# Performance work log

Measured on AMD Instinct MI355X. Metric: run time of the kernel, lower is better.

The kernel has to match this reference:

```python
import jax, jax.numpy as jnp
import numpy as np

# dims: batch B, seq S, model D, query heads H, kv heads KV, head_dim HD, group G
B, S, D = 2, 2048, 2048
H, KV, HD = 16, 4, 128
G = H // KV
THETA = 10000.0


def setup_inputs() -> dict:
    key = jax.random.key(0)
    ks = jax.random.split(key, 5)
    x = jax.random.normal(ks[0], (B, S, D), dtype=jnp.float32)
    # RoPE frequencies (real/imag parts of complex freqs_cis)
    inv_freq = 1.0 / (THETA ** (jnp.arange(0, HD, 2, dtype=jnp.float32) / HD))  # (HD/2,)
    t = jnp.arange(S, dtype=jnp.float32)
    freqs = jnp.outer(t, inv_freq)                      # (S, HD/2)
    freqs_cos = jnp.cos(freqs)
    freqs_sin = jnp.sin(freqs)
    # causal additive mask
    mask = jnp.where(jnp.tril(jnp.ones((S, S), dtype=bool)), 0.0, -1e9).astype(jnp.float32)
    sc = 0.02
    wq = jax.random.normal(ks[1], (D, H * HD), dtype=jnp.float32) * sc
    wk = jax.random.normal(ks[2], (D, KV * HD), dtype=jnp.float32) * sc
    wv = jax.random.normal(ks[3], (D, KV * HD), dtype=jnp.float32) * sc
    wo = jax.random.normal(ks[4], (H * HD, D), dtype=jnp.float32) * sc
    return {"x": x, "freqs_cos": freqs_cos, "freqs_sin": freqs_sin, "mask": mask,
            "wq": wq, "wk": wk, "wv": wv, "wo": wo}


def _apply_rope(x, cos, sin):
    # x: (B, S, nh, HD); cos/sin: (S, HD/2). Interleaved complex rotation.
    xr = x.reshape(*x.shape[:-1], HD // 2, 2)
    xe, xo = xr[..., 0], xr[..., 1]
    c = cos[None, :, None, :]
    s = sin[None, :, None, :]
    out_e = xe * c - xo * s
    out_o = xe * s + xo * c
    return jnp.stack([out_e, out_o], axis=-1).reshape(x.shape)


def reference(x, freqs_cos, freqs_sin, mask, wq, wk, wv, wo):
    q = (x @ wq).reshape(B, S, H, HD)
    k = (x @ wk).reshape(B, S, KV, HD)
    v = (x @ wv).reshape(B, S, KV, HD)
    q = _apply_rope(q, freqs_cos, freqs_sin)
    k = _apply_rope(k, freqs_cos, freqs_sin)
    # GQA: group query heads instead of expanding KV (same math as expand)
    qg = q.reshape(B, S, KV, G, HD)
    scale = jnp.sqrt(jnp.float32(HD))
    scores = jnp.einsum('bqkgd,bskd->bkgqs', qg, k) / scale   # (B,KV,G,S,S)
    scores = scores + mask                                     # broadcast (S,S)
    attn = jax.nn.softmax(scores, axis=-1)
    out = jnp.einsum('bkgqs,bskd->bqkgd', attn, v)             # (B,S,KV,G,HD)
    out = out.reshape(B, S, H * HD)
    return out @ wo
```

## Files before the change

### kernel.cpp

```cpp
#include <hip/hip_runtime.h>
#include <type_traits>

typedef short s8v   __attribute__((ext_vector_type(8)));
typedef float f32x4 __attribute__((ext_vector_type(4)));
typedef float f32x16 __attribute__((ext_vector_type(16)));
typedef unsigned int u32x2 __attribute__((ext_vector_type(2)));
typedef unsigned int u32x4 __attribute__((ext_vector_type(4)));

__device__ __forceinline__ unsigned short f2bf(float f) {
    unsigned int u = __builtin_bit_cast(unsigned int, f);
    u += 0x7FFF + ((u >> 16) & 1);
    return (unsigned short)(u >> 16);
}
__device__ __forceinline__ float bf2f(unsigned short b) {
    unsigned int u = ((unsigned int)b) << 16;
    return __builtin_bit_cast(float, u);
}
__device__ __forceinline__ unsigned int cvtpk(float lo, float hi) {
    unsigned int w;
    asm("v_cvt_pk_bf16_f32 %0, %1, %2" : "=v"(w) : "v"(lo), "v"(hi));
    return w;
}

__device__ __forceinline__ void gload16(const void* g, void* l) {
    __builtin_amdgcn_global_load_lds(
        (const __attribute__((address_space(1))) void*)g,
        (__attribute__((address_space(3))) void*)l, 16, 0, 0);
}

__global__ __launch_bounds__(256)
void prep_kernel(const float* __restrict__ x, const float* __restrict__ wq,
                 const float* __restrict__ wk, const float* __restrict__ wv,
                 const float* __restrict__ wo,
                 unsigned short* __restrict__ xb, unsigned short* __restrict__ wqkvT,
                 unsigned short* __restrict__ woT) {
    __shared__ float tile[32][33];
    const int bid = blockIdx.x;
    if (bid < 4096) {
        int i = bid * 256 + threadIdx.x;
        const f32x4* s4 = (const f32x4*)x;
        f32x4 a = s4[2 * i], b = s4[2 * i + 1];
        s8v o;
        o[0] = (short)f2bf(a[0]); o[1] = (short)f2bf(a[1]);
        o[2] = (short)f2bf(a[2]); o[3] = (short)f2bf(a[3]);
        o[4] = (short)f2bf(b[0]); o[5] = (short)f2bf(b[1]);
        o[6] = (short)f2bf(b[2]); o[7] = (short)f2bf(b[3]);
        *(s8v*)(xb + (size_t)i * 8) = o;
        return;
    }
    const int tx = threadIdx.x & 31, ty = threadIdx.x >> 5;
    const float* src; unsigned short* dst; int sc, N, n0, k0;
    if (bid < 10240) {
        int lb = bid - 4096;
        n0 = (lb % 96) * 32; k0 = (lb / 96) * 32;
        if (n0 < 2048)      { src = wq; sc = n0;        N = 2048; }
        else if (n0 < 2560) { src = wk; sc = n0 - 2048; N = 512;  }
        else                { src = wv; sc = n0 - 2560; N = 512;  }
        dst = wqkvT;
    } else {
        int lb = bid - 10240;
        n0 = (lb % 64) * 32; k0 = (lb / 64) * 32;
        src = wo; sc = n0; N = 2048; dst = woT;
    }
#pragma unroll
    for (int r = 0; r < 4; ++r)
        tile[ty + r * 8][tx] = src[(size_t)(k0 + ty + r * 8) * N + sc + tx];
    __syncthreads();
#pragma unroll
    for (int r = 0; r < 4; ++r)
        dst[(size_t)(n0 + ty + r * 8) * 2048 + k0 + tx] = f2bf(tile[tx][ty + r * 8]);
}

__global__ void rope_kernel(unsigned short* __restrict__ qkv,
                            const float* __restrict__ fc, const float* __restrict__ fs) {
    int idx = blockIdx.x * blockDim.x + threadIdx.x;
    if (idx >= 4096 * 20 * 16) return;
    int grp = idx & 15;
    int hh = (idx >> 4) % 20;
    int row = idx / (16 * 20);
    int s = row & 2047;
    int col0 = (hh < 16 ? hh * 128 : 2048 + (hh - 16) * 128) + grp * 8;
    unsigned short* p = qkv + (size_t)row * 3072 + col0;
    s8v v = *(const s8v*)p;
    const float* cc = fc + (size_t)s * 64 + grp * 4;
    const float* ss = fs + (size_t)s * 64 + grp * 4;
    const float sc = (hh < 16) ? 0.08838834764831845f : 1.0f;
#pragma unroll
    for (int j = 0; j < 4; ++j) {
        float xe = bf2f((unsigned short)v[2 * j]);
        float xo = bf2f((unsigned short)v[2 * j + 1]);
        float c = cc[j], sn = ss[j];
        v[2 * j]     = (short)f2bf((xe * c - xo * sn) * sc);
        v[2 * j + 1] = (short)f2bf((xe * sn + xo * c) * sc);
    }
    *(s8v*)p = v;
}

__global__ void vtrans(const unsigned short* __restrict__ qkv, unsigned short* __restrict__ vt) {
    __shared__ unsigned short t[32][33];
    int s0 = blockIdx.x * 32;
    int c0 = blockIdx.y * 32;
    int tx = threadIdx.x, ty = threadIdx.y;
#pragma unroll
    for (int r = 0; r < 4; ++r)
        t[ty + r * 8][tx] = qkv[(size_t)(s0 + ty + r * 8) * 3072 + 2560 + c0 + tx];
    __syncthreads();
    int b = s0 >> 11, s = s0 & 2047;
    size_t dbase = (size_t)(b * 4 + (c0 >> 7)) * 128 + (c0 & 127);
#pragma unroll
    for (int r = 0; r < 4; ++r)
        vt[(dbase + ty + r * 8) * 2048 + s + tx] = t[tx][ty + r * 8];
}

template <typename CT>
__global__ __launch_bounds__(256)
void gemm_bt(const unsigned short* __restrict__ A, const unsigned short* __restrict__ BT,
             CT* __restrict__ C, int M, int N, int K, int ldc) {
    __shared__ unsigned short As[128 * 64];
    __shared__ unsigned short Bs[128 * 64];
    const int tid = threadIdx.x;
    const int wid = tid >> 6, lane = tid & 63;
    const int l31 = lane & 31, h2 = lane >> 5;
    const int nbx = N >> 7;
    const int per = nbx >> 3;
    const int xcd = blockIdx.x & 7;
    const int li  = blockIdx.x >> 3;
    const int bx  = xcd * per + (li % per);
    const int by  = li / per;
    const int brow = by * 128, bcol = bx * 128;
    const int wr = wid >> 1, wc = wid & 1;
    f32x16 acc[2][2] = {};

    for (int kt = 0; kt < K; kt += 64) {
#pragma unroll
        for (int i = 0; i < 4; ++i) {
            int c = i * 256 + tid;
            int row = c >> 3, u = c & 7;
            gload16(A + (size_t)(brow + row) * K + kt + ((u ^ (row & 7)) << 3),
                    As + (size_t)c * 8);
            gload16(BT + (size_t)(bcol + row) * K + kt + ((u ^ (row & 7)) << 3),
                    Bs + (size_t)c * 8);
        }
        __syncthreads();
        s8v a[2][4], b[2][4];
#pragma unroll
        for (int mm = 0; mm < 2; ++mm) {
            int row = wr * 64 + mm * 32 + l31;
#pragma unroll
            for (int ks = 0; ks < 4; ++ks)
                a[mm][ks] = *(const s8v*)(As + (size_t)row * 64 +
                                          (((2 * ks + h2) ^ (row & 7)) << 3));
        }
#pragma unroll
        for (int nn = 0; nn < 2; ++nn) {
            int row = wc * 64 + nn * 32 + l31;
#pragma unroll
            for (int ks = 0; ks < 4; ++ks)
                b[nn][ks] = *(const s8v*)(Bs + (size_t)row * 64 +
                                          (((2 * ks + h2) ^ (row & 7)) << 3));
        }
#pragma unroll
        for (int ks = 0; ks < 4; ++ks)
#pragma unroll
            for (int mm = 0; mm < 2; ++mm)
#pragma unroll
                for (int nn = 0; nn < 2; ++nn)
                    acc[mm][nn] = __builtin_amdgcn_mfma_f32_32x32x16_bf16(
                        a[mm][ks], b[nn][ks], acc[mm][nn], 0, 0, 0);
        __syncthreads();
    }
#pragma unroll
    for (int mm = 0; mm < 2; ++mm)
#pragma unroll
        for (int nn = 0; nn < 2; ++nn)
#pragma unroll
            for (int reg = 0; reg < 16; ++reg) {
                int r = brow + wr * 64 + mm * 32 + (reg & 3) + 8 * (reg >> 2) + 4 * h2;
                int c = bcol + wc * 64 + nn * 32 + l31;
                float v = acc[mm][nn][reg];
                if constexpr (std::is_same<CT, float>::value)
                    C[(size_t)r * ldc + c] = v;
                else
                    C[(size_t)r * ldc + c] = f2bf(v);
            }
}

__global__ __launch_bounds__(256)
void attn_kernel(const unsigned short* __restrict__ qkv,
                 const unsigned short* __restrict__ vtg,
                 unsigned short* __restrict__ out) {
    constexpr int S = 2048;
    __shared__ unsigned short Ks[2][64 * 128];
    __shared__ unsigned short Vs[2][128 * 64];
    const int tid = threadIdx.x, lane = tid & 63, wid = tid >> 6;
    const int l31 = lane & 31, h2 = lane >> 5;
    const int lsw = l31 & 7;
    const int g8 = blockIdx.x & 7;
    const int b = g8 >> 2, kvh = g8 & 3;
    const int qi = 63 - (blockIdx.x >> 3);
    const int h = kvh * 4 + wid;
    const int qw = qi * 32;
    const int qq = qw + l31;
    const size_t rs = 3072;

    const unsigned short* Qp = qkv + (size_t)(b * S + qw) * rs + h * 128 + h2 * 8;
    const unsigned short* Kbase = qkv + (size_t)(b * S) * rs + 2048 + kvh * 128;
    const unsigned short* Vtg = vtg + (size_t)((b * 4 + kvh) * 128) * S;

    s8v qf[8];
#pragma unroll
    for (int kk = 0; kk < 8; ++kk)
        qf[kk] = *(const s8v*)(Qp + (size_t)l31 * rs + kk * 16);

    f32x16 acc[4] = {};
    float m_run = -1e30f, l_run = 0.f;
    const int nt = (qi >> 1) + 1;

    auto stage = [&](int t, int bufi) {
        const int kb64 = t * 64;
#pragma unroll
        for (int i = 0; i < 4; ++i) {
            int c = i * 256 + tid;
            int key = c >> 4, d8 = c & 15;
            gload16(Kbase + (size_t)(kb64 + key) * rs + ((d8 ^ (key & 7)) << 3),
                    &Ks[bufi][(size_t)c * 8]);
        }
#pragma unroll
        for (int i = 0; i < 4; ++i) {
            int c = i * 256 + tid;
            int d = c >> 3, k8 = c & 7;
            gload16(Vtg + (size_t)d * S + kb64 + ((k8 ^ (d & 7)) << 3),
                    &Vs[bufi][(size_t)c * 8]);
        }
    };

    int cur = 0;
    stage(0, 0);
    __syncthreads();

    for (int t = 0; t < nt; ++t) {
        if (t + 1 < nt) stage(t + 1, cur ^ 1);
        const int kb64 = t * 64;
        const char* Kb = (const char*)&Ks[cur][0];
        const char* Vb = (const char*)&Vs[cur][0];

        s8v kf0[8], kf1[8];
#pragma unroll
        for (int kk = 0; kk < 8; ++kk)
            kf0[kk] = *(const s8v*)(Kb + l31 * 256 + (((2 * kk + h2) ^ lsw) << 4));
#pragma unroll
        for (int kk = 0; kk < 8; ++kk)
            kf1[kk] = *(const s8v*)(Kb + (32 + l31) * 256 + (((2 * kk + h2) ^ lsw) << 4));
        s8v vf[4][4];
#pragma unroll
        for (int kb = 0; kb < 4; ++kb)
#pragma unroll
            for (int dblk = 0; dblk < 4; ++dblk)
                vf[kb][dblk] = *(const s8v*)(Vb + (32 * dblk + l31) * 128 +
                                             (((2 * kb + h2) ^ lsw) << 4));

        f32x16 sacc0 = {}, sacc1 = {};
        __builtin_amdgcn_s_setprio(1);
#pragma unroll
        for (int kk = 0; kk < 8; ++kk)
            sacc0 = __builtin_amdgcn_mfma_f32_32x32x16_bf16(kf0[kk], qf[kk], sacc0, 0, 0, 0);
#pragma unroll
        for (int kk = 0; kk < 8; ++kk)
            sacc1 = __builtin_amdgcn_mfma_f32_32x32x16_bf16(kf1[kk], qf[kk], sacc1, 0, 0, 0);
        __builtin_amdgcn_s_setprio(0);

        float sv[32];
        if (t == nt - 1) {
#pragma unroll
            for (int g = 0; g < 2; ++g)
#pragma unroll
                for (int r = 0; r < 16; ++r) {
                    int key = kb64 + 32 * g + (r & 3) + 8 * (r >> 2) + 4 * h2;
                    float s = (g ? sacc1[r] : sacc0[r]);
                    sv[g * 16 + r] = (key <= qq) ? s : -1e30f;
                }
        } else {
#pragma unroll
            for (int r = 0; r < 16; ++r) sv[r] = sacc0[r];
#pragma unroll
            for (int r = 0; r < 16; ++r) sv[16 + r] = sacc1[r];
        }

        float mx = sv[0];
#pragma unroll
        for (int i = 1; i < 32; ++i) mx = fmaxf(mx, sv[i]);
        mx = fmaxf(mx, __shfl_xor(mx, 32));
        if (!__all(mx - m_run <= 8.f)) {
            float mn = fmaxf(m_run, mx);
            float alpha = __expf(m_run - mn);
            m_run = mn;
            l_run *= alpha;
#pragma unroll
            for (int dblk = 0; dblk < 4; ++dblk)
#pragma unroll
                for (int r = 0; r < 16; ++r) acc[dblk][r] *= alpha;
        }
        float ps = 0.f;
#pragma unroll
        for (int i = 0; i < 32; ++i) {
            float e = __expf(sv[i] - m_run);
            sv[i] = e;
            ps += e;
        }
        ps += __shfl_xor(ps, 32);
        l_run += ps;

        unsigned int pw[4][4];
#pragma unroll
        for (int g = 0; g < 2; ++g) {
            unsigned int w[8];
#pragma unroll
            for (int j = 0; j < 8; ++j)
                w[j] = cvtpk(sv[g * 16 + 2 * j], sv[g * 16 + 2 * j + 1]);
#pragma unroll
            for (int u = 0; u < 2; ++u) {
                unsigned int t0 = (unsigned)__shfl_xor((int)w[4 * u + 0], 32);
                unsigned int t1 = (unsigned)__shfl_xor((int)w[4 * u + 1], 32);
                unsigned int t2 = (unsigned)__shfl_xor((int)w[4 * u + 2], 32);
                unsigned int t3 = (unsigned)__shfl_xor((int)w[4 * u + 3], 32);
                pw[2 * g + u][0] = h2 ? t2 : w[4 * u + 0];
                pw[2 * g + u][1] = h2 ? t3 : w[4 * u + 1];
                pw[2 * g + u][2] = h2 ? w[4 * u + 2] : t0;
                pw[2 * g + u][3] = h2 ? w[4 * u + 3] : t1;
            }
        }

        __builtin_amdgcn_s_setprio(1);
#pragma unroll
        for (int kb = 0; kb < 4; ++kb) {
            u32x4 wv;
            wv[0] = pw[kb][0]; wv[1] = pw[kb][1]; wv[2] = pw[kb][2]; wv[3] = pw[kb][3];
            s8v pf = __builtin_bit_cast(s8v, wv);
#pragma unroll
            for (int dblk = 0; dblk < 4; ++dblk)
                acc[dblk] = __builtin_amdgcn_mfma_f32_32x32x16_bf16(vf[kb][dblk], pf, acc[dblk], 0, 0, 0);
        }
        __builtin_amdgcn_s_setprio(0);

        __syncthreads();
        cur ^= 1;
    }

    float inv = 1.f / l_run;
    unsigned short* Op = out + (size_t)(b * S + qq) * 2048 + h * 128 + 4 * h2;
#pragma unroll
    for (int dblk = 0; dblk < 4; ++dblk)
#pragma unroll
        for (int s = 0; s < 4; ++s) {
            u32x2 wv;
            wv[0] = cvtpk(acc[dblk][4 * s + 0] * inv, acc[dblk][4 * s + 1] * inv);
            wv[1] = cvtpk(acc[dblk][4 * s + 2] * inv, acc[dblk][4 * s + 3] * inv);
            *(u32x2*)(Op + 32 * dblk + 8 * s) = wv;
        }
}

extern "C" void kernel_launch(void* const* d_in, const int* in_sizes, int n_in,
                              void* d_out, int out_size, void* d_ws, size_t ws_size,
                              hipStream_t stream) {
    const float* x  = (const float*)d_in[0];
    const float* fc = (const float*)d_in[1];
    const float* fs = (const float*)d_in[2];
    const float* wq = (const float*)d_in[4];
    const float* wk = (const float*)d_in[5];
    const float* wv = (const float*)d_in[6];
    const float* wo = (const float*)d_in[7];
    float* out = (float*)d_out;

    char* ws = (char*)d_ws;
    unsigned short* xb    = (unsigned short*)ws;
    unsigned short* wqkvT = (unsigned short*)(ws + 16777216);
    unsigned short* woT   = (unsigned short*)(ws + 16777216 + 12582912);
    unsigned short* qkvb  = (unsigned short*)(ws + 16777216 + 12582912 + 8388608);
    unsigned short* attnb = xb;
    unsigned short* vtb   = wqkvT;

    prep_kernel<<<14336, 256, 0, stream>>>(x, wq, wk, wv, wo, xb, wqkvT, woT);
    gemm_bt<unsigned short><<<768, 256, 0, stream>>>(
        xb, wqkvT, qkvb, 4096, 3072, 2048, 3072);
    rope_kernel<<<5120, 256, 0, stream>>>(qkvb, fc, fs);
    dim3 tb(32, 8);
    vtrans<<<dim3(128, 16), tb, 0, stream>>>(qkvb, vtb);
    attn_kernel<<<512, 256, 0, stream>>>(qkvb, vtb, attnb);
    gemm_bt<float><<<512, 256, 0, stream>>>(
        attnb, woT, out, 4096, 2048, 2048, 2048);
}
```

Measured before the change: 220.8 us.

## Split long causal attention blocks across KV, merge partials, fuse RoPE with V transpose

Query blocks in the upper half of the causal range have their KV loop split into two halves, each run by a separate block. Those blocks write unnormalized fp32 partial outputs plus (max, sum) pairs into scratch, and a new merge kernel combines the two halves. The aim is to fix load imbalance, since the longest query blocks otherwise dominate the attention tail. RoPE and the V transpose now run in one launch to save a kernel launch. Softmax switches to exp2 with log2(e) folded into the Q scale, and the rescale threshold is widened. This costs an extra kernel and extra fp32 scratch traffic, reusing the output buffer as scratch.

After: 256.0 us. 15.9% more time.

```diff
diff --git a/kernel.cpp b/kernel.cpp
--- a/kernel.cpp
+++ b/kernel.cpp
@@ -71,36 +71,37 @@
         dst[(size_t)(n0 + ty + r * 8) * 2048 + k0 + tx] = f2bf(tile[tx][ty + r * 8]);
 }
 
-__global__ void rope_kernel(unsigned short* __restrict__ qkv,
-                            const float* __restrict__ fc, const float* __restrict__ fs) {
-    int idx = blockIdx.x * blockDim.x + threadIdx.x;
-    if (idx >= 4096 * 20 * 16) return;
-    int grp = idx & 15;
-    int hh = (idx >> 4) % 20;
-    int row = idx / (16 * 20);
-    int s = row & 2047;
-    int col0 = (hh < 16 ? hh * 128 : 2048 + (hh - 16) * 128) + grp * 8;
-    unsigned short* p = qkv + (size_t)row * 3072 + col0;
-    s8v v = *(const s8v*)p;
-    const float* cc = fc + (size_t)s * 64 + grp * 4;
-    const float* ss = fs + (size_t)s * 64 + grp * 4;
-    const float sc = (hh < 16) ? 0.08838834764831845f : 1.0f;
-#pragma unroll
-    for (int j = 0; j < 4; ++j) {
-        float xe = bf2f((unsigned short)v[2 * j]);
-        float xo = bf2f((unsigned short)v[2 * j + 1]);
-        float c = cc[j], sn = ss[j];
-        v[2 * j]     = (short)f2bf((xe * c - xo * sn) * sc);
-        v[2 * j + 1] = (short)f2bf((xe * sn + xo * c) * sc);
-    }
-    *(s8v*)p = v;
-}
-
-__global__ void vtrans(const unsigned short* __restrict__ qkv, unsigned short* __restrict__ vt) {
+__global__ __launch_bounds__(256)
+void ropevt_kernel(unsigned short* __restrict__ qkv, const float* __restrict__ fc,
+                   const float* __restrict__ fs, unsigned short* __restrict__ vt) {
     __shared__ unsigned short t[32][33];
-    int s0 = blockIdx.x * 32;
-    int c0 = blockIdx.y * 32;
-    int tx = threadIdx.x, ty = threadIdx.y;
+    const int bid = blockIdx.x;
+    if (bid < 5120) {
+        int idx = bid * 256 + threadIdx.x;
+        int grp = idx & 15;
+        int hh = (idx >> 4) % 20;
+        int row = idx / (16 * 20);
+        int s = row & 2047;
+        int col0 = (hh < 16 ? hh * 128 : 2048 + (hh - 16) * 128) + grp * 8;
+        unsigned short* p = qkv + (size_t)row * 3072 + col0;
+        s8v v = *(const s8v*)p;
+        const float* cc = fc + (size_t)s * 64 + grp * 4;
+        const float* ss = fs + (size_t)s * 64 + grp * 4;
+        const float sc = (hh < 16) ? (0.08838834764831845f * 1.4426950408889634f) : 1.0f;
+#pragma unroll
+        for (int j = 0; j < 4; ++j) {
+            float xe = bf2f((unsigned short)v[2 * j]);
+            float xo = bf2f((unsigned short)v[2 * j + 1]);
+            float c = cc[j], sn = ss[j];
+            v[2 * j]     = (short)f2bf((xe * c - xo * sn) * sc);
+            v[2 * j + 1] = (short)f2bf((xe * sn + xo * c) * sc);
+        }
+        *(s8v*)p = v;
+        return;
+    }
+    int vb = bid - 5120;
+    int s0 = (vb & 127) * 32, c0 = (vb >> 7) * 32;
+    int tx = threadIdx.x & 31, ty = threadIdx.x >> 5;
 #pragma unroll
     for (int r = 0; r < 4; ++r)
         t[ty + r * 8][tx] = qkv[(size_t)(s0 + ty + r * 8) * 3072 + 2560 + c0 + tx];
@@ -188,16 +189,29 @@
 __global__ __launch_bounds__(256)
 void attn_kernel(const unsigned short* __restrict__ qkv,
                  const unsigned short* __restrict__ vtg,
-                 unsigned short* __restrict__ out) {
+                 unsigned short* __restrict__ out,
+                 float* __restrict__ opart, float* __restrict__ ml) {
     constexpr int S = 2048;
     __shared__ unsigned short Ks[2][64 * 128];
     __shared__ unsigned short Vs[2][128 * 64];
     const int tid = threadIdx.x, lane = tid & 63, wid = tid >> 6;
     const int l31 = lane & 31, h2 = lane >> 5;
     const int lsw = l31 & 7;
-    const int g8 = blockIdx.x & 7;
+
+    const int u = blockIdx.x;
+    int qi, g8, t0, t1, half = 0, split = 0;
+    if (u < 512) {
+        int pair = u >> 1; half = u & 1; split = 1;
+        qi = 63 - (pair >> 3); g8 = pair & 7;
+        int ntf0 = (qi >> 1) + 1, nth = ntf0 >> 1;
+        t0 = half ? nth : 0; t1 = half ? ntf0 : nth;
+    } else {
+        int v2 = u - 512;
+        qi = 31 - (v2 >> 3); g8 = v2 & 7;
+        t0 = 0; t1 = (qi >> 1) + 1;
+    }
+    const int ntf = (qi >> 1) + 1;
     const int b = g8 >> 2, kvh = g8 & 3;
-    const int qi = 63 - (blockIdx.x >> 3);
     const int h = kvh * 4 + wid;
     const int qw = qi * 32;
     const int qq = qw + l31;
@@ -214,7 +228,6 @@
 
     f32x16 acc[4] = {};
     float m_run = -1e30f, l_run = 0.f;
-    const int nt = (qi >> 1) + 1;
 
     auto stage = [&](int t, int bufi) {
         const int kb64 = t * 64;
@@ -235,11 +248,11 @@
     };
 
     int cur = 0;
-    stage(0, 0);
+    stage(t0, 0);
     __syncthreads();
 
-    for (int t = 0; t < nt; ++t) {
-        if (t + 1 < nt) stage(t + 1, cur ^ 1);
+    for (int t = t0; t < t1; ++t) {
+        if (t + 1 < t1) stage(t + 1, cur ^ 1);
         const int kb64 = t * 64;
         const char* Kb = (const char*)&Ks[cur][0];
         const char* Vb = (const char*)&Vs[cur][0];
@@ -270,7 +283,7 @@
         __builtin_amdgcn_s_setprio(0);
 
         float sv[32];
-        if (t == nt - 1) {
+        if (t == ntf - 1) {
 #pragma unroll
             for (int g = 0; g < 2; ++g)
 #pragma unroll
@@ -290,9 +303,9 @@
 #pragma unroll
         for (int i = 1; i < 32; ++i) mx = fmaxf(mx, sv[i]);
         mx = fmaxf(mx, __shfl_xor(mx, 32));
-        if (!__all(mx - m_run <= 8.f)) {
+        if (!__all(mx - m_run <= 11.5f)) {
             float mn = fmaxf(m_run, mx);
-            float alpha = __expf(m_run - mn);
+            float alpha = exp2f(m_run - mn);
             m_run = mn;
             l_run *= alpha;
 #pragma unroll
@@ -303,7 +316,7 @@
         float ps = 0.f;
 #pragma unroll
         for (int i = 0; i < 32; ++i) {
-            float e = __expf(sv[i] - m_run);
+            float e = exp2f(sv[i] - m_run);
             sv[i] = e;
             ps += e;
         }
@@ -318,15 +331,15 @@
             for (int j = 0; j < 8; ++j)
                 w[j] = cvtpk(sv[g * 16 + 2 * j], sv[g * 16 + 2 * j + 1]);
 #pragma unroll
-            for (int u = 0; u < 2; ++u) {
-                unsigned int t0 = (unsigned)__shfl_xor((int)w[4 * u + 0], 32);
-                unsigned int t1 = (unsigned)__shfl_xor((int)w[4 * u + 1], 32);
-                unsigned int t2 = (unsigned)__shfl_xor((int)w[4 * u + 2], 32);
-                unsigned int t3 = (unsigned)__shfl_xor((int)w[4 * u + 3], 32);
-                pw[2 * g + u][0] = h2 ? t2 : w[4 * u + 0];
-                pw[2 * g + u][1] = h2 ? t3 : w[4 * u + 1];
-                pw[2 * g + u][2] = h2 ? w[4 * u + 2] : t0;
-                pw[2 * g + u][3] = h2 ? w[4 * u + 3] : t1;
+            for (int uu = 0; uu < 2; ++uu) {
+                unsigned int t0w = (unsigned)__shfl_xor((int)w[4 * uu + 0], 32);
+                unsigned int t1w = (unsigned)__shfl_xor((int)w[4 * uu + 1], 32);
+                unsigned int t2w = (unsigned)__shfl_xor((int)w[4 * uu + 2], 32);
+                unsigned int t3w = (unsigned)__shfl_xor((int)w[4 * uu + 3], 32);
+                pw[2 * g + uu][0] = h2 ? t2w : w[4 * uu + 0];
+                pw[2 * g + uu][1] = h2 ? t3w : w[4 * uu + 1];
+                pw[2 * g + uu][2] = h2 ? w[4 * uu + 2] : t0w;
+                pw[2 * g + uu][3] = h2 ? w[4 * uu + 3] : t1w;
             }
         }
 
@@ -346,17 +359,75 @@
         cur ^= 1;
     }
 
-    float inv = 1.f / l_run;
-    unsigned short* Op = out + (size_t)(b * S + qq) * 2048 + h * 128 + 4 * h2;
-#pragma unroll
-    for (int dblk = 0; dblk < 4; ++dblk)
-#pragma unroll
-        for (int s = 0; s < 4; ++s) {
-            u32x2 wv;
-            wv[0] = cvtpk(acc[dblk][4 * s + 0] * inv, acc[dblk][4 * s + 1] * inv);
-            wv[1] = cvtpk(acc[dblk][4 * s + 2] * inv, acc[dblk][4 * s + 3] * inv);
-            *(u32x2*)(Op + 32 * dblk + 8 * s) = wv;
-        }
+    if (split) {
+        const int p = ((g8 * 4 + wid) * 32 + (qi - 32)) * 2 + half;
+        float* Op = opart + ((size_t)p * 32 + l31) * 128 + 4 * h2;
+#pragma unroll
+        for (int dblk = 0; dblk < 4; ++dblk)
+#pragma unroll
+            for (int s = 0; s < 4; ++s) {
+                f32x4 v;
+                v[0] = acc[dblk][4 * s + 0]; v[1] = acc[dblk][4 * s + 1];
+                v[2] = acc[dblk][4 * s + 2]; v[3] = acc[dblk][4 * s + 3];
+                *(f32x4*)(Op + 32 * dblk + 8 * s) = v;
+            }
+        if (h2 == 0) {
+            float2* ml2 = (float2*)ml;
+            ml2[p * 32 + l31] = make_float2(m_run, l_run);
+        }
+    } else {
+        float inv = 1.f / l_run;
+        unsigned short* Opb = out + (size_t)(b * S + qq) * 2048 + h * 128 + 4 * h2;
+#pragma unroll
+        for (int dblk = 0; dblk < 4; ++dblk)
+#pragma unroll
+            for (int s = 0; s < 4; ++s) {
+                u32x2 wv;
+                wv[0] = cvtpk(acc[dblk][4 * s + 0] * inv, acc[dblk][4 * s + 1] * inv);
+                wv[1] = cvtpk(acc[dblk][4 * s + 2] * inv, acc[dblk][4 * s + 3] * inv);
+                *(u32x2*)(Opb + 32 * dblk + 8 * s) = wv;
+            }
+    }
+}
+
+__global__ __launch_bounds__(256)
+void attn_merge(const float* __restrict__ opart, const float* __restrict__ ml,
+                unsigned short* __restrict__ out) {
+    const int mb = blockIdx.x;
+    const int g8h = mb & 31;
+    const int qi = 32 + (mb >> 5);
+    const int g8 = g8h >> 2, hsub = g8h & 3;
+    const int b = g8 >> 2, kvh = g8 & 3;
+    const int h = kvh * 4 + hsub;
+    const int p0 = (g8h * 32 + (qi - 32)) * 2, p1 = p0 + 1;
+    const int tid = threadIdx.x;
+    const int q = tid >> 3, d0 = (tid & 7) * 16;
+
+    const float2* ml2 = (const float2*)ml;
+    float2 a = ml2[p0 * 32 + q], c = ml2[p1 * 32 + q];
+    float m = fmaxf(a.x, c.x);
+    float w1 = exp2f(a.x - m), w2 = exp2f(c.x - m);
+    float inv = 1.f / (w1 * a.y + w2 * c.y);
+    w1 *= inv; w2 *= inv;
+    const float* O0 = opart + ((size_t)p0 * 32 + q) * 128 + d0;
+    const float* O1 = opart + ((size_t)p1 * 32 + q) * 128 + d0;
+    unsigned int r[8];
+#pragma unroll
+    for (int i = 0; i < 4; ++i) {
+        f32x4 v0 = *(const f32x4*)(O0 + 4 * i);
+        f32x4 v1 = *(const f32x4*)(O1 + 4 * i);
+        float x0 = w1 * v0[0] + w2 * v1[0];
+        float x1 = w1 * v0[1] + w2 * v1[1];
+        float x2 = w1 * v0[2] + w2 * v1[2];
+        float x3 = w1 * v0[3] + w2 * v1[3];
+        r[2 * i]     = cvtpk(x0, x1);
+        r[2 * i + 1] = cvtpk(x2, x3);
+    }
+    unsigned short* Ob = out + (size_t)(b * 2048 + qi * 32 + q) * 2048 + h * 128 + d0;
+    u32x4 w0; w0[0] = r[0]; w0[1] = r[1]; w0[2] = r[2]; w0[3] = r[3];
+    u32x4 w1v; w1v[0] = r[4]; w1v[1] = r[5]; w1v[2] = r[6]; w1v[3] = r[7];
+    *(u32x4*)Ob = w0;
+    *(u32x4*)(Ob + 8) = w1v;
 }
 
 extern "C" void kernel_launch(void* const* d_in, const int* in_sizes, int n_in,
@@ -378,14 +449,15 @@
     unsigned short* qkvb  = (unsigned short*)(ws + 16777216 + 12582912 + 8388608);
     unsigned short* attnb = xb;
     unsigned short* vtb   = wqkvT;
+    float* mlbuf = (float*)(ws + 16777216 + 4194304);
+    float* opart = out;
 
     prep_kernel<<<14336, 256, 0, stream>>>(x, wq, wk, wv, wo, xb, wqkvT, woT);
     gemm_bt<unsigned short><<<768, 256, 0, stream>>>(
         xb, wqkvT, qkvb, 4096, 3072, 2048, 3072);
-    rope_kernel<<<5120, 256, 0, stream>>>(qkvb, fc, fs);
-    dim3 tb(32, 8);
-    vtrans<<<dim3(128, 16), tb, 0, stream>>>(qkvb, vtb);
-    attn_kernel<<<512, 256, 0, stream>>>(qkvb, vtb, attnb);
+    ropevt_kernel<<<7168, 256, 0, stream>>>(qkvb, fc, fs, vtb);
+    attn_kernel<<<768, 256, 0, stream>>>(qkvb, vtb, attnb, opart, mlbuf);
+    attn_merge<<<1024, 256, 0, stream>>>(opart, mlbuf, attnb);
     gemm_bt<float><<<512, 256, 0, stream>>>(
         attnb, woT, out, 4096, 2048, 2048, 2048);
 }
```
